# Performance work log

Hardware: AMD Instinct MI355X
Metric: run time of the kernel (lower is better)

## Reference

```python
import jax, jax.numpy as jnp
import numpy as np
from jax.scipy.fft import dct as jdct, idct as jidct

B, C, L = 512, 64, 512
KEEP_L, KEEP_C = 256, 32          # int(L*0.5), int(C*0.5)
KEEP_L2, KEEP_C2 = 128, 16        # int(KEEP_L*0.5), int(KEEP_C*0.5)


def dct2(x2d):
    # scipy: dct(dct(x, axis=0, norm='ortho'), axis=1, norm='ortho') on (B*C, L)
    return jdct(jdct(x2d, norm='ortho', axis=0), norm='ortho', axis=1)


def idct2(x2d):
    # scipy: idct(idct(X, axis=1, norm='ortho'), axis=0, norm='ortho')
    return jidct(jidct(x2d, norm='ortho', axis=1), norm='ortho', axis=0)


def setup_inputs() -> dict:
    key = jax.random.key(0)
    ks = jax.random.split(key, 7)
    x = jax.random.normal(ks[0], (B, C, L), dtype=jnp.float32)
    W1 = jax.random.normal(ks[1], (L, L), dtype=jnp.float32) / np.sqrt(L)
    b1 = jax.random.normal(ks[2], (L,), dtype=jnp.float32) * 0.01
    W2 = jax.random.normal(ks[3], (KEEP_L, KEEP_L), dtype=jnp.float32) / np.sqrt(KEEP_L)
    b2 = jax.random.normal(ks[4], (KEEP_L,), dtype=jnp.float32) * 0.01
    W3 = jax.random.normal(ks[5], (KEEP_L2, KEEP_L2), dtype=jnp.float32) / np.sqrt(KEEP_L2)
    b3 = jax.random.normal(ks[6], (KEEP_L2,), dtype=jnp.float32) * 0.01
    return {"x": x, "W1": W1, "b1": b1, "W2": W2, "b2": b2, "W3": W3, "b3": b3}


def reference(x, W1, b1, W2, b2, W3, b3):
    Bx, Cx, Lx = x.shape
    # 2D DCT over the flattened (B*C, L) view
    T = dct2(x.reshape(-1, Lx)).reshape(Bx, Cx, Lx)

    # branch 1: Linear over full L
    y1 = T @ W1.T + b1

    # branch 2: Linear over truncated coeffs, zero-pad back to (B, C, L)
    t1 = T[:, :KEEP_C, :KEEP_L]
    y2 = jnp.pad(t1 @ W2.T + b2, ((0, 0), (0, Cx - KEEP_C), (0, Lx - KEEP_L)))

    # branch 3: further truncation
    t2 = T[:, :KEEP_C2, :KEEP_L2]
    y3 = jnp.pad(t2 @ W3.T + b3, ((0, 0), (0, Cx - KEEP_C2), (0, Lx - KEEP_L2)))

    out = jnp.concatenate(
        [idct2(y.reshape(-1, Lx)).reshape(Bx, Cx, Lx) for y in (y1, y2, y3)],
        axis=-1,
    )  # (B, C, 3L)
    return out
```

## Files before the change

### kernel.cpp

```cpp
#include <hip/hip_runtime.h>
#include <cstddef>


#define PI_D 3.14159265358979323846

typedef _Float16 h8 __attribute__((ext_vector_type(8)));
typedef _Float16 h4 __attribute__((ext_vector_type(4)));
typedef float f4 __attribute__((ext_vector_type(4)));

#define MFMA16(a, b, c) __builtin_amdgcn_mfma_f32_16x16x32_f16(a, b, c, 0, 0, 0)

__global__ __launch_bounds__(256) void megafill_k(
    float* __restrict__ F, _Float16* __restrict__ Cmh, _Float16* __restrict__ Smnh,
    _Float16* __restrict__ CmTh, _Float16* __restrict__ SmTh,
    float* __restrict__ v1, float* __restrict__ w2, float* __restrict__ w3,
    const float* __restrict__ b1, const float* __restrict__ b2,
    const float* __restrict__ b3, float* __restrict__ c1, float* __restrict__ c2,
    float* __restrict__ c3) {
  const int blk = blockIdx.x;
  const int tid = threadIdx.x;
  if (blk < 1024) {
    int idx = blk * 256 + tid;
    int k = idx >> 9, m = idx & 511;
    int a = (k * (2 * m + 1)) & 2047;
    float ang = (float)(a * (PI_D / 1024.0));
    float s = (k == 0) ? 0.04419417382415922f : 0.0625f;
    F[idx] = s * cosf(ang);
  } else if (blk < 2048) {
    int idx = (blk - 1024) * 256 + tid;
    int t = idx >> 9, v = idx & 511;
    int a = (t * (2 * v + 1)) & 2047;
    float ang = (float)(a * (PI_D / 1024.0));
    float c = cosf(ang), s = sinf(ang);
    Cmh[idx] = (_Float16)c;
    Smnh[idx] = (_Float16)(-s);
    CmTh[v * 512 + t] = (_Float16)c;
    SmTh[v * 512 + t] = (_Float16)s;
  } else if (blk < 2176) {
    int n = (blk - 2048) * 256 + tid;
    const double s1 = 0.005524271728019903;
    const double s2 = 0.0078125;
    double th = (2 * n + 1) * (PI_D / 65536.0);
    double c = cos(th), s = sin(th);
    double Dr = 1.0 - c, Di = -s;
    double dd = Dr * Dr + Di * Di;
    double Nr = 1.0, Ni = (n & 1) ? 1.0 : -1.0;
    double vre = (Nr * Dr + Ni * Di) / dd;
    v1[n] = (float)(s2 * vre + (s1 - s2));
    int m64 = (2 * n + 1) & 2047;
    double a64 = m64 * (PI_D / 1024.0);
    double D64r = 1.0 - cos(a64), D64i = -sin(a64);
    double d64 = D64r * D64r + D64i * D64i;
    double Gr = (Nr * D64r + Ni * D64i) / d64;
    double Gi = (Ni * D64r - Nr * D64i) / d64;
    int m32 = (2 * n + 1) & 4095;
    double a32 = m32 * (PI_D / 2048.0);
    double S32nr = 1.0 - cos(a32), S32ni = -sin(a32);
    double S32r = (S32nr * Dr + S32ni * Di) / dd;
    double S32i = (S32ni * Dr - S32nr * Di) / dd;
    w2[n] = (float)(s2 * (S32r * Gr - S32i * Gi) + (s1 - s2));
    int m16 = (2 * n + 1) & 8191;
    double a16 = m16 * (PI_D / 4096.0);
    double S16nr = 1.0 - cos(a16), S16ni = -sin(a16);
    double S16r = (S16nr * Dr + S16ni * Di) / dd;
    double S16i = (S16ni * Dr - S16nr * Di) / dd;
    w3[n] = (float)(s2 * (S16r * Gr - S16i * Gi) + (s1 - s2));
  } else {
    int gid = (blk - 2176) * 4 + (tid >> 6);
    int lane = tid & 63;
    int branch = gid >> 9;
    int l = gid & 511;
    int K = 512 >> branch;
    const float* b = (branch == 0) ? b1 : (branch == 1) ? b2 : b3;
    float acc = 0.f;
    for (int m = lane; m < K; m += 64) {
      int a = (m * (2 * l + 1)) & 2047;
      float s = (m == 0) ? 0.04419417382415922f : 0.0625f;
      acc += s * cosf((float)(a * (PI_D / 1024.0))) * b[m];
    }
#pragma unroll
    for (int o = 32; o > 0; o >>= 1) acc += __shfl_down(acc, o, 64);
    if (lane == 0) {
      float* c = (branch == 0) ? c1 : (branch == 1) ? c2 : c3;
      c[l] = acc;
    }
  }
}

__global__ void conv_xh_k(const float* __restrict__ X, _Float16* __restrict__ Xh) {
  int i = blockIdx.x * 256 + threadIdx.x;
  float4 v = ((const float4*)X)[i];
  h4 o;
  o[0] = (_Float16)v.x; o[1] = (_Float16)v.y; o[2] = (_Float16)v.z; o[3] = (_Float16)v.w;
  ((h4*)Xh)[i] = o;
}

__device__ void sgemm_dev(_Float16* As, _Float16* Bs, int bx, int by,
                          const float* __restrict__ A, int lda, int transA,
                          const float* __restrict__ B, int ldb,
                          float* __restrict__ Cf, _Float16* __restrict__ C16,
                          int K, float scale) {
  const int tid = threadIdx.x;
  const int lane = tid & 63;
  const int wm = (tid >> 6) & 1, wn = tid >> 7;
  const int m0 = by * 128, n0 = bx * 128;
  const int fm = lane & 15, fko = (lane >> 4) * 8;
  f4 acc[4][4] = {};
  for (int k0 = 0; k0 < K; k0 += 32) {
    if (transA) {
#pragma unroll
      for (int i = 0; i < 4; i++) {
        int idx4 = tid + i * 256;
        int kk = idx4 & 31, mc = (idx4 >> 5) * 4;
        float4 v = *(const float4*)&A[(size_t)(k0 + kk) * lda + m0 + mc];
        As[(mc + 0) * 40 + kk] = (_Float16)v.x;
        As[(mc + 1) * 40 + kk] = (_Float16)v.y;
        As[(mc + 2) * 40 + kk] = (_Float16)v.z;
        As[(mc + 3) * 40 + kk] = (_Float16)v.w;
      }
    } else {
#pragma unroll
      for (int i = 0; i < 4; i++) {
        int idx4 = tid + i * 256;
        int mm = idx4 >> 3, kc = (idx4 & 7) * 4;
        float4 v = *(const float4*)&A[(size_t)(m0 + mm) * lda + k0 + kc];
        h4 o;
        o[0] = (_Float16)v.x; o[1] = (_Float16)v.y; o[2] = (_Float16)v.z; o[3] = (_Float16)v.w;
        *(h4*)&As[mm * 40 + kc] = o;
      }
    }
#pragma unroll
    for (int i = 0; i < 4; i++) {
      int idx4 = tid + i * 256;
      int kk = idx4 & 31, nc = (idx4 >> 5) * 4;
      float4 v = *(const float4*)&B[(size_t)(k0 + kk) * ldb + n0 + nc];
      Bs[(nc + 0) * 40 + kk] = (_Float16)v.x;
      Bs[(nc + 1) * 40 + kk] = (_Float16)v.y;
      Bs[(nc + 2) * 40 + kk] = (_Float16)v.z;
      Bs[(nc + 3) * 40 + kk] = (_Float16)v.w;
    }
    __syncthreads();
    h8 af[4], bf[4];
#pragma unroll
    for (int i = 0; i < 4; i++) af[i] = *(const h8*)&As[(wm * 64 + i * 16 + fm) * 40 + fko];
#pragma unroll
    for (int j = 0; j < 4; j++) bf[j] = *(const h8*)&Bs[(wn * 64 + j * 16 + fm) * 40 + fko];
#pragma unroll
    for (int i = 0; i < 4; i++)
#pragma unroll
      for (int j = 0; j < 4; j++) acc[i][j] = MFMA16(af[i], bf[j], acc[i][j]);
    __syncthreads();
  }
  const int er = (lane >> 4) * 4, ec = lane & 15;
#pragma unroll
  for (int i = 0; i < 4; i++) {
    int gr0 = m0 + wm * 64 + i * 16 + er;
#pragma unroll
    for (int j = 0; j < 4; j++) {
      int gc = n0 + wn * 64 + j * 16 + ec;
#pragma unroll
      for (int r = 0; r < 4; r++) {
        size_t off = (size_t)(gr0 + r) * 512 + gc;
        if (C16) C16[off] = (_Float16)(acc[i][j][r] * scale);
        else Cf[off] = acc[i][j][r];
      }
    }
  }
}

__global__ __launch_bounds__(256) void sgemm_stage1_k(
    const float* __restrict__ W1, const float* __restrict__ W2,
    const float* __restrict__ W3, const float* __restrict__ F,
    float* __restrict__ Pst, float* __restrict__ Q2, float* __restrict__ Q3) {
  __shared__ _Float16 As[128 * 40];
  __shared__ _Float16 Bs[128 * 40];
  int id = blockIdx.x;
  if (id < 16) {
    sgemm_dev(As, Bs, id & 3, id >> 2, W1, 512, 1, F, 512, Pst, nullptr, 512, 1.f);
  } else if (id < 24) {
    int j = id - 16;
    sgemm_dev(As, Bs, j & 3, j >> 2, W2, 256, 0, F, 512, Q2, nullptr, 256, 1.f);
  } else {
    int j = id - 24;
    sgemm_dev(As, Bs, j & 3, j >> 2, W3, 128, 0, F, 512, Q3, nullptr, 128, 1.f);
  }
}

__global__ __launch_bounds__(256) void sgemm_stage2_k(
    const float* __restrict__ F, const float* __restrict__ Pst,
    const float* __restrict__ Q2, const float* __restrict__ Q3,
    _Float16* __restrict__ M1T, _Float16* __restrict__ M2T,
    _Float16* __restrict__ M3T) {
  __shared__ _Float16 As[128 * 40];
  __shared__ _Float16 Bs[128 * 40];
  int id = blockIdx.x;
  if (id < 16) {
    sgemm_dev(As, Bs, id & 3, id >> 2, Pst, 512, 1, F, 512, nullptr, M1T, 512, 1.f);
  } else if (id < 32) {
    int j = id - 16;
    sgemm_dev(As, Bs, j & 3, j >> 2, F, 512, 1, Q2, 512, nullptr, M2T, 256, 0.0078125f);
  } else {
    int j = id - 32;
    sgemm_dev(As, Bs, j & 3, j >> 2, F, 512, 1, Q3, 512, nullptr, M3T, 128, 0.0078125f);
  }
}

__global__ __launch_bounds__(256) void transpose2_h_k(
    const _Float16* __restrict__ in0, _Float16* __restrict__ out0, int C0,
    const _Float16* __restrict__ in1, _Float16* __restrict__ out1, int C1,
    int xsplit, int R) {
  __shared__ _Float16 t[64][66];
  const _Float16* in;
  _Float16* out;
  int C, bx;
  if ((int)blockIdx.x < xsplit) { in = in0; out = out0; C = C0; bx = blockIdx.x; }
  else { in = in1; out = out1; C = C1; bx = blockIdx.x - xsplit; }
  int tid = threadIdx.x;
  int bxo = bx * 64;
  int by = blockIdx.y * 64;
  int cx = (tid & 15) * 4;
  int ry = tid >> 4;
#pragma unroll
  for (int p = 0; p < 4; p++) {
    int r = ry + p * 16;
    h4 v = *(const h4*)&in[(size_t)(by + r) * C + bxo + cx];
    t[r][cx + 0] = v[0]; t[r][cx + 1] = v[1]; t[r][cx + 2] = v[2]; t[r][cx + 3] = v[3];
  }
  __syncthreads();
#pragma unroll
  for (int p = 0; p < 4; p++) {
    int r2 = ry + p * 16;
    h4 v;
    v[0] = t[cx + 0][r2]; v[1] = t[cx + 1][r2]; v[2] = t[cx + 2][r2]; v[3] = t[cx + 3][r2];
    *(h4*)&out[(size_t)(bxo + r2) * R + by + cx] = v;
  }
}

__device__ __forceinline__ void async16(const _Float16* g, _Float16* l) {
  __builtin_amdgcn_global_load_lds((const __attribute__((address_space(1))) void*)g,
                                   (__attribute__((address_space(3))) void*)l, 16, 0, 0);
}

template <int MODE>
__device__ void gemm_dev(_Float16* As, _Float16* Bs, int bx, int by,
                         const _Float16* __restrict__ A1, const _Float16* __restrict__ A2,
                         const _Float16* __restrict__ B1, const _Float16* __restrict__ B2,
                         void* __restrict__ C1, void* __restrict__ C2, int ldc, int coff,
                         const float* __restrict__ u, const float* __restrict__ wvec,
                         int sb, int tb) {
  constexpr bool DA = (MODE == 1 || MODE == 2);
  constexpr bool DB = (MODE == 1);
  const int tid = threadIdx.x;
  const int lane = tid & 63;
  const int wm = (tid >> 6) & 1, wn = tid >> 7;
  const int m0 = by * 128, n0 = bx * 128;
  const int srow = tid >> 2, scol = (tid & 3) * 8;
  const int mask = (1 << sb) - 1;
  f4 acc[4][4] = {};
  f4 acc2[4][4] = {};
  const int fm = lane & 15, fko = (lane >> 4) * 8;
  for (int k0 = 0; k0 < 512; k0 += 32) {
#pragma unroll
    for (int i = 0; i < 2; i++) {
      int r = m0 + i * 64 + srow;
      int pr = ((r >> sb) << tb) | (r & mask);
      async16(A1 + (size_t)pr * 512 + k0 + scol, &As[i * 2048 + tid * 8]);
      if constexpr (DA)
        async16(A2 + (size_t)pr * 512 + k0 + scol, &As[4096 + i * 2048 + tid * 8]);
      int rb = n0 + i * 64 + srow;
      async16(B1 + (size_t)rb * 512 + k0 + scol, &Bs[i * 2048 + tid * 8]);
      if constexpr (DB)
        async16(B2 + (size_t)rb * 512 + k0 + scol, &Bs[4096 + i * 2048 + tid * 8]);
    }
    __syncthreads();
    h8 af[4], bf[4], af2[4], bf2[4];
#pragma unroll
    for (int i = 0; i < 4; i++) {
      int ro = (wm * 64 + i * 16 + fm) * 32 + fko;
      af[i] = *(const h8*)&As[ro];
      if constexpr (DA) af2[i] = *(const h8*)&As[4096 + ro];
    }
#pragma unroll
    for (int j = 0; j < 4; j++) {
      int co = (wn * 64 + j * 16 + fm) * 32 + fko;
      bf[j] = *(const h8*)&Bs[co];
      if constexpr (DB) bf2[j] = *(const h8*)&Bs[4096 + co];
    }
#pragma unroll
    for (int i = 0; i < 4; i++)
#pragma unroll
      for (int j = 0; j < 4; j++) {
        acc[i][j] = MFMA16(af[i], bf[j], acc[i][j]);
        if constexpr (MODE == 1) acc[i][j] = MFMA16(af2[i], bf2[j], acc[i][j]);
        if constexpr (MODE == 2) acc2[i][j] = MFMA16(af2[i], bf[j], acc2[i][j]);
      }
    __syncthreads();
  }
  const int er = (lane >> 4) * 4, ec = lane & 15;
#pragma unroll
  for (int i = 0; i < 4; i++) {
    int gr0 = m0 + wm * 64 + i * 16 + er;
#pragma unroll
    for (int j = 0; j < 4; j++) {
      int gc = n0 + wn * 64 + j * 16 + ec;
#pragma unroll
      for (int r = 0; r < 4; r++) {
        size_t off = (size_t)(gr0 + r) * ldc + coff + gc;
        if constexpr (MODE == 3) {
          ((float*)C1)[off] = acc[i][j][r] + u[gr0 + r] * wvec[gc];
        } else if constexpr (MODE == 2) {
          ((_Float16*)C1)[off] = (_Float16)acc[i][j][r];
          ((_Float16*)C2)[off] = (_Float16)acc2[i][j][r];
        } else if constexpr (MODE == 1) {
          float v = acc[i][j][r];
          if ((gr0 + r) == 0 && gc < 512) v *= 0.5f;
          ((_Float16*)C1)[off] = (_Float16)v;
        } else {
          ((_Float16*)C1)[off] = (_Float16)acc[i][j][r];
        }
      }
    }
  }
}

template <int MODE>
__global__ __launch_bounds__(256) void mfma_gemm_k(
    const _Float16* __restrict__ A1, const _Float16* __restrict__ A2,
    const _Float16* __restrict__ B1, const _Float16* __restrict__ B2,
    void* __restrict__ C1, void* __restrict__ C2, int ldc, int coff,
    const float* __restrict__ u, const float* __restrict__ wvec, int sb, int tb) {
  __shared__ __align__(16) _Float16 As[((MODE == 1 || MODE == 2) ? 2 : 1) * 4096];
  __shared__ __align__(16) _Float16 Bs[(MODE == 1 ? 2 : 1) * 4096];
  gemm_dev<MODE>(As, Bs, blockIdx.x, blockIdx.y, A1, A2, B1, B2, C1, C2, ldc, coff,
                 u, wvec, sb, tb);
}

__global__ __launch_bounds__(256) void gemm_trio_k(
    const _Float16* __restrict__ Zh, const _Float16* __restrict__ M2T,
    const _Float16* __restrict__ M3T, _Float16* __restrict__ Y2,
    _Float16* __restrict__ Y3, const _Float16* __restrict__ Xh,
    const _Float16* __restrict__ M1T, float* __restrict__ out,
    const float* __restrict__ v1, const float* __restrict__ c1) {
  __shared__ __align__(16) _Float16 As[4096];
  __shared__ __align__(16) _Float16 Bs[4096];
  int by = blockIdx.y;
  if (by < 128)
    gemm_dev<0>(As, Bs, blockIdx.x, by, Zh, nullptr, M2T, nullptr, Y2, nullptr,
                512, 0, nullptr, nullptr, 30, 30);
  else if (by < 192)
    gemm_dev<0>(As, Bs, blockIdx.x, by - 128, Zh, nullptr, M3T, nullptr, Y3,
                nullptr, 512, 0, nullptr, nullptr, 4, 5);
  else
    gemm_dev<3>(As, Bs, blockIdx.x, by - 192, Xh, nullptr, M1T, nullptr, out,
                nullptr, 1536, 0, v1, c1, 30, 30);
}

__global__ __launch_bounds__(256) void gemm2_pair_k(
    const _Float16* __restrict__ CmTh, const _Float16* __restrict__ SmTh,
    const _Float16* __restrict__ Y2T, const _Float16* __restrict__ Y3T,
    _Float16* __restrict__ Pc2, _Float16* __restrict__ Ps2,
    _Float16* __restrict__ Pc3, _Float16* __restrict__ Ps3) {
  __shared__ __align__(16) _Float16 As[2 * 4096];
  __shared__ __align__(16) _Float16 Bs[4096];
  if ((int)blockIdx.x < 128)
    gemm_dev<2>(As, Bs, blockIdx.x, blockIdx.y, CmTh, SmTh, Y2T, nullptr, Pc2, Ps2,
                16384, 0, nullptr, nullptr, 30, 30);
  else
    gemm_dev<2>(As, Bs, blockIdx.x - 128, blockIdx.y, CmTh, SmTh, Y3T, nullptr, Pc3,
                Ps3, 8192, 0, nullptr, nullptr, 30, 30);
}

__global__ __launch_bounds__(256) void modmfma_k(
    const _Float16* __restrict__ Xh, _Float16* __restrict__ zc,
    _Float16* __restrict__ zs) {
  __shared__ _Float16 Bs[256 * 72];
  __shared__ _Float16 Ac[32 * 72];
  __shared__ _Float16 As[32 * 72];
  const int tid = threadIdx.x;
  const int lane = tid & 63;
  const int wid = tid >> 6;
  const int vp = blockIdx.y;
  const int l0 = blockIdx.x * 256;
  const float sc = 0.0078125f;
  {
    int r = lane;
    int u = r & 31;
    int n = (r < 32) ? ((u << 10) + vp) : ((u << 10) + 1023 - vp);
    const _Float16* src = Xh + (size_t)n * 512 + l0 + wid * 64;
#pragma unroll
    for (int i = 0; i < 8; i++) {
      h8 v = *(const h8*)(src + i * 8);
      int lb = wid * 64 + i * 8;
#pragma unroll
      for (int e = 0; e < 8; e++) Bs[(lb + e) * 72 + r] = v[e];
    }
  }
  for (int idx = tid; idx < 2048; idx += 256) {
    int kk = idx & 63, j = idx >> 6;
    int u = kk & 31;
    int n = (kk < 32) ? ((u << 10) + vp) : ((u << 10) + 1023 - vp);
    int a = (j * (2 * n + 1)) & 131071;
    float sv, cv;
    __sincosf((float)(a * (PI_D / 65536.0)), &sv, &cv);
    Ac[j * 72 + kk] = (_Float16)(cv * sc);
    As[j * 72 + kk] = (_Float16)(((kk < 32) ? sv : -sv) * sc);
  }
  __syncthreads();
  const int fm = lane & 15, fko = (lane >> 4) * 8;
  f4 accc[2][4] = {};
  f4 accs[2][4] = {};
#pragma unroll
  for (int ks = 0; ks < 2; ks++) {
    int ko = ks * 32 + fko;
    h8 afc[2], afs[2], bf[4];
#pragma unroll
    for (int i = 0; i < 2; i++) {
      afc[i] = *(const h8*)&Ac[(i * 16 + fm) * 72 + ko];
      afs[i] = *(const h8*)&As[(i * 16 + fm) * 72 + ko];
    }
#pragma unroll
    for (int j = 0; j < 4; j++)
      bf[j] = *(const h8*)&Bs[(wid * 64 + j * 16 + fm) * 72 + ko];
#pragma unroll
    for (int i = 0; i < 2; i++)
#pragma unroll
      for (int j = 0; j < 4; j++) {
        accc[i][j] = MFMA16(afc[i], bf[j], accc[i][j]);
        accs[i][j] = MFMA16(afs[i], bf[j], accs[i][j]);
      }
  }
  const int er = (lane >> 4) * 4, ec = lane & 15;
#pragma unroll
  for (int i = 0; i < 2; i++)
#pragma unroll
    for (int j = 0; j < 4; j++)
#pragma unroll
      for (int r = 0; r < 4; r++) {
        int row = i * 16 + er + r;
        int col = l0 + wid * 64 + j * 16 + ec;
        size_t off = (size_t)vp * 16384 + row * 512 + col;
        zc[off] = (_Float16)accc[i][j][r];
        zs[off] = (_Float16)accs[i][j][r];
      }
}

template <int JC>
__device__ void demod_dev(char* smemraw, const _Float16* __restrict__ Pc,
                          const _Float16* __restrict__ Ps,
                          const float* __restrict__ wv, const float* __restrict__ cw,
                          float* __restrict__ out, int coff) {
  constexpr int K2 = 2 * JC;
  constexpr int ST = K2 + 8;
  _Float16* Bs = (_Float16*)smemraw;
  _Float16* At = (_Float16*)(smemraw + (size_t)256 * ST * 2);
  const int tid = threadIdx.x;
  const int lane = tid & 63;
  const int wid = tid >> 6;
  const int vp = blockIdx.y;
  const int l0 = blockIdx.x * 256;
  {
    constexpr int CPL = 64 / K2;
    int r = lane & (K2 - 1);
    int chunk = wid * CPL + (CPL == 1 ? 0 : (lane >> 5));
    int lb = chunk * K2;
    const _Float16* src = (r < JC ? Pc + (size_t)vp * (JC * 512) + r * 512
                                  : Ps + (size_t)vp * (JC * 512) + (r - JC) * 512) +
                          l0 + lb;
#pragma unroll
    for (int i = 0; i < K2 / 8; i++) {
      h8 v = *(const h8*)(src + i * 8);
#pragma unroll
      for (int e = 0; e < 8; e++) Bs[(lb + i * 8 + e) * ST + r] = v[e];
    }
  }
  for (int idx = tid; idx < 64 * K2; idx += 256) {
    int kk = idx & (K2 - 1), m = idx / K2;
    int ab = m >> 5, u = m & 31;
    int n = ab ? ((u << 10) + 1023 - vp) : ((u << 10) + vp);
    int twon = 2 * n + 1;
    float val;
    if (kk < JC) {
      int a = (kk * twon) & 131071;
      val = cosf((float)(a * (PI_D / 65536.0)));
    } else {
      int a = ((kk - JC) * twon) & 131071;
      float sv = sinf((float)(a * (PI_D / 65536.0)));
      val = ab ? sv : -sv;
    }
    At[m * ST + kk] = (_Float16)val;
  }
  __syncthreads();
  const int fm = lane & 15, fko = (lane >> 4) * 8;
  f4 acc[4][4] = {};
#pragma unroll
  for (int ks = 0; ks < K2 / 32; ks++) {
    int ko = ks * 32 + fko;
    h8 af[4], bf[4];
#pragma unroll
    for (int i = 0; i < 4; i++) af[i] = *(const h8*)&At[(i * 16 + fm) * ST + ko];
#pragma unroll
    for (int j = 0; j < 4; j++) bf[j] = *(const h8*)&Bs[(wid * 64 + j * 16 + fm) * ST + ko];
#pragma unroll
    for (int i = 0; i < 4; i++)
#pragma unroll
      for (int j = 0; j < 4; j++) acc[i][j] = MFMA16(af[i], bf[j], acc[i][j]);
  }
  const int er = (lane >> 4) * 4, ec = lane & 15;
#pragma unroll
  for (int i = 0; i < 4; i++)
#pragma unroll
    for (int j = 0; j < 4; j++) {
      int col = l0 + wid * 64 + j * 16 + ec;
      float cl = cw[col];
#pragma unroll
      for (int r = 0; r < 4; r++) {
        int m = i * 16 + er + r;
        int ab = m >> 5, u = m & 31;
        int n = ab ? ((u << 10) + 1023 - vp) : ((u << 10) + vp);
        out[(size_t)n * 1536 + coff + col] = acc[i][j][r] + wv[n] * cl;
      }
    }
}

__global__ __launch_bounds__(256) void demod_pair_k(
    const _Float16* __restrict__ Pc2, const _Float16* __restrict__ Ps2,
    const float* __restrict__ w2v, const float* __restrict__ c2,
    const _Float16* __restrict__ Pc3, const _Float16* __restrict__ Ps3,
    const float* __restrict__ w3v, const float* __restrict__ c3,
    float* __restrict__ out) {
  __shared__ __align__(16) char smem[256 * 72 * 2 + 64 * 72 * 2];
  if (blockIdx.z == 0)
    demod_dev<32>(smem, Pc2, Ps2, w2v, c2, out, 512);
  else
    demod_dev<16>(smem, Pc3, Ps3, w3v, c3, out, 1024);
}

extern "C" void kernel_launch(void* const* d_in, const int* in_sizes, int n_in,
                              void* d_out, int out_size, void* d_ws, size_t ws_size,
                              hipStream_t stream) {
  const float* X  = (const float*)d_in[0];
  const float* W1 = (const float*)d_in[1];
  const float* b1 = (const float*)d_in[2];
  const float* W2 = (const float*)d_in[3];
  const float* b2 = (const float*)d_in[4];
  const float* W3 = (const float*)d_in[5];
  const float* b3 = (const float*)d_in[6];
  float* out = (float*)d_out;
  char* w = (char*)d_ws;
  const size_t MB = 1024 * 1024;

  float* F    = (float*)(w);
  float* v1   = (float*)(w + 9 * MB);
  float* w2v  = (float*)(w + 9 * MB + 131072);
  float* w3v  = (float*)(w + 9 * MB + 262144);
  float* c1   = (float*)(w + 9 * MB + 393216);
  float* c2   = (float*)(w + 9 * MB + 395264);
  float* c3   = (float*)(w + 9 * MB + 397312);
  float* Pst  = (float*)(w + 10 * MB);
  _Float16* CmTh = (_Float16*)(w + 11 * MB);
  _Float16* SmTh = (_Float16*)(w + 11 * MB + 524288);
  _Float16* Cmh  = (_Float16*)(w + 12 * MB);
  _Float16* Smnh = (_Float16*)(w + 12 * MB + 524288);
  _Float16* M1T  = (_Float16*)(w + 13 * MB);
  _Float16* M2T  = (_Float16*)(w + 13 * MB + 524288);
  _Float16* M3T  = (_Float16*)(w + 14 * MB);
  float* Q2      = (float*)(w + 14 * MB + 524288);
  float* Q3      = (float*)(w + 15 * MB);
  _Float16* Xh   = (_Float16*)(w + 16 * MB);
  _Float16* zc   = (_Float16*)(w + 48 * MB);
  _Float16* zs   = (_Float16*)(w + 64 * MB);
  _Float16* Pc2h = (_Float16*)(w + 48 * MB);
  _Float16* Ps2h = (_Float16*)(w + 64 * MB);
  _Float16* Pc3h = (_Float16*)(w + 104 * MB);
  _Float16* Ps3h = (_Float16*)(w + 112 * MB);
  _Float16* zcT  = (_Float16*)(w + 80 * MB);
  _Float16* zsT  = (_Float16*)(w + 96 * MB);
  _Float16* Y2T  = (_Float16*)(w + 80 * MB);
  _Float16* Y3T  = (_Float16*)(w + 96 * MB);
  _Float16* Zh   = (_Float16*)(w + 112 * MB);
  _Float16* Y2   = (_Float16*)(w + 128 * MB);
  _Float16* Y3   = (_Float16*)(w + 144 * MB);

  megafill_k<<<2560, 256, 0, stream>>>(F, Cmh, Smnh, CmTh, SmTh, v1, w2v, w3v,
                                       b1, b2, b3, c1, c2, c3);
  sgemm_stage1_k<<<28, 256, 0, stream>>>(W1, W2, W3, F, Pst, Q2, Q3);
  sgemm_stage2_k<<<48, 256, 0, stream>>>(F, Pst, Q2, Q3, M1T, M2T, M3T);
  conv_xh_k<<<16384, 256, 0, stream>>>(X, Xh);
  modmfma_k<<<dim3(2, 512), 256, 0, stream>>>(Xh, zc, zs);
  transpose2_h_k<<<dim3(512, 8), 256, 0, stream>>>(zc, zcT, 16384, zs, zsT, 16384,
                                                   256, 512);
  mfma_gemm_k<1><<<dim3(128, 4), 256, 0, stream>>>(Cmh, Smnh, zcT, zsT, Zh, nullptr,
                                                   16384, 0, nullptr, nullptr, 30, 30);
  gemm_trio_k<<<dim3(4, 448), 256, 0, stream>>>(Zh, M2T, M3T, Y2, Y3, Xh, M1T, out,
                                                v1, c1);
  transpose2_h_k<<<dim3(384, 8), 256, 0, stream>>>(Y2, Y2T, 16384, Y3, Y3T, 8192,
                                                   256, 512);
  gemm2_pair_k<<<dim3(192, 4), 256, 0, stream>>>(CmTh, SmTh, Y2T, Y3T, Pc2h, Ps2h,
                                                 Pc3h, Ps3h);
  demod_pair_k<<<dim3(2, 512, 2), 256, 0, stream>>>(Pc2h, Ps2h, w2v, c2, Pc3h, Ps3h,
                                                    w3v, c3, out);
}
```

Before: 584.6 us.

## Fuse fp16 conversion into modulation MFMA and co-launch stage-2 sgemm blocks

Drops the standalone float-to-half conversion kernel: the modulation kernel now reads fp32 X directly, converts it in registers, writes Xh for later use and stages it to shared memory. The stage-2 weight sgemm blocks are merged into the same launch as extra blocks, so those independent tasks share one grid and two launches go away. The aim is to cut the extra read of Xh and kernel launch overhead. The fused kernel reads twice as many bytes per element from X and uses a union shared buffer sized for the larger path, which may lower occupancy for the sgemm blocks.

```diff
diff --git a/kernel.cpp b/kernel.cpp
--- a/kernel.cpp
+++ b/kernel.cpp
@@ -87,14 +87,6 @@
   }
 }
 
-__global__ void conv_xh_k(const float* __restrict__ X, _Float16* __restrict__ Xh) {
-  int i = blockIdx.x * 256 + threadIdx.x;
-  float4 v = ((const float4*)X)[i];
-  h4 o;
-  o[0] = (_Float16)v.x; o[1] = (_Float16)v.y; o[2] = (_Float16)v.z; o[3] = (_Float16)v.w;
-  ((h4*)Xh)[i] = o;
-}
-
 __device__ void sgemm_dev(_Float16* As, _Float16* Bs, int bx, int by,
                           const float* __restrict__ A, int lda, int transA,
                           const float* __restrict__ B, int ldb,
@@ -186,22 +178,108 @@
   }
 }
 
-__global__ __launch_bounds__(256) void sgemm_stage2_k(
+__device__ void modmfma_dev(char* smemraw, const float* __restrict__ X,
+                            _Float16* __restrict__ Xh, _Float16* __restrict__ zc,
+                            _Float16* __restrict__ zs, int vp, int l0) {
+  _Float16* Bs = (_Float16*)smemraw;
+  _Float16* Ac = (_Float16*)(smemraw + 36864);
+  _Float16* As = (_Float16*)(smemraw + 41472);
+  const int tid = threadIdx.x;
+  const int lane = tid & 63;
+  const int wid = tid >> 6;
+  const float sc = 0.0078125f;
+  {
+    int r = lane;
+    int u = r & 31;
+    int n = (r < 32) ? ((u << 10) + vp) : ((u << 10) + 1023 - vp);
+    const float* src = X + (size_t)n * 512 + l0 + wid * 64;
+    _Float16* xdst = Xh + (size_t)n * 512 + l0 + wid * 64;
+#pragma unroll
+    for (int i = 0; i < 8; i++) {
+      float4 a = *(const float4*)(src + i * 8);
+      float4 b = *(const float4*)(src + i * 8 + 4);
+      h8 v;
+      v[0] = (_Float16)a.x; v[1] = (_Float16)a.y; v[2] = (_Float16)a.z; v[3] = (_Float16)a.w;
+      v[4] = (_Float16)b.x; v[5] = (_Float16)b.y; v[6] = (_Float16)b.z; v[7] = (_Float16)b.w;
+      *(h8*)(xdst + i * 8) = v;
+      int lb = wid * 64 + i * 8;
+#pragma unroll
+      for (int e = 0; e < 8; e++) Bs[(lb + e) * 72 + r] = v[e];
+    }
+  }
+  for (int idx = tid; idx < 2048; idx += 256) {
+    int kk = idx & 63, j = idx >> 6;
+    int u = kk & 31;
+    int n = (kk < 32) ? ((u << 10) + vp) : ((u << 10) + 1023 - vp);
+    int a = (j * (2 * n + 1)) & 131071;
+    float sv, cv;
+    __sincosf((float)(a * (PI_D / 65536.0)), &sv, &cv);
+    Ac[j * 72 + kk] = (_Float16)(cv * sc);
+    As[j * 72 + kk] = (_Float16)(((kk < 32) ? sv : -sv) * sc);
+  }
+  __syncthreads();
+  const int fm = lane & 15, fko = (lane >> 4) * 8;
+  f4 accc[2][4] = {};
+  f4 accs[2][4] = {};
+#pragma unroll
+  for (int ks = 0; ks < 2; ks++) {
+    int ko = ks * 32 + fko;
+    h8 afc[2], afs[2], bf[4];
+#pragma unroll
+    for (int i = 0; i < 2; i++) {
+      afc[i] = *(const h8*)&Ac[(i * 16 + fm) * 72 + ko];
+      afs[i] = *(const h8*)&As[(i * 16 + fm) * 72 + ko];
+    }
+#pragma unroll
+    for (int j = 0; j < 4; j++)
+      bf[j] = *(const h8*)&Bs[(wid * 64 + j * 16 + fm) * 72 + ko];
+#pragma unroll
+    for (int i = 0; i < 2; i++)
+#pragma unroll
+      for (int j = 0; j < 4; j++) {
+        accc[i][j] = MFMA16(afc[i], bf[j], accc[i][j]);
+        accs[i][j] = MFMA16(afs[i], bf[j], accs[i][j]);
+      }
+  }
+  const int er = (lane >> 4) * 4, ec = lane & 15;
+#pragma unroll
+  for (int i = 0; i < 2; i++)
+#pragma unroll
+    for (int j = 0; j < 4; j++)
+#pragma unroll
+      for (int r = 0; r < 4; r++) {
+        int row = i * 16 + er + r;
+        int col = l0 + wid * 64 + j * 16 + ec;
+        size_t off = (size_t)vp * 16384 + row * 512 + col;
+        zc[off] = (_Float16)accc[i][j][r];
+        zs[off] = (_Float16)accs[i][j][r];
+      }
+}
+
+__global__ __launch_bounds__(256) void mega3_k(
+    const float* __restrict__ X, _Float16* __restrict__ Xh,
+    _Float16* __restrict__ zc, _Float16* __restrict__ zs,
     const float* __restrict__ F, const float* __restrict__ Pst,
     const float* __restrict__ Q2, const float* __restrict__ Q3,
     _Float16* __restrict__ M1T, _Float16* __restrict__ M2T,
     _Float16* __restrict__ M3T) {
-  __shared__ _Float16 As[128 * 40];
-  __shared__ _Float16 Bs[128 * 40];
-  int id = blockIdx.x;
-  if (id < 16) {
-    sgemm_dev(As, Bs, id & 3, id >> 2, Pst, 512, 1, F, 512, nullptr, M1T, 512, 1.f);
-  } else if (id < 32) {
-    int j = id - 16;
-    sgemm_dev(As, Bs, j & 3, j >> 2, F, 512, 1, Q2, 512, nullptr, M2T, 256, 0.0078125f);
+  __shared__ __align__(16) char smem[46080];
+  const int blk = blockIdx.x;
+  if (blk < 1024) {
+    modmfma_dev(smem, X, Xh, zc, zs, blk >> 1, (blk & 1) * 256);
   } else {
-    int j = id - 32;
-    sgemm_dev(As, Bs, j & 3, j >> 2, F, 512, 1, Q3, 512, nullptr, M3T, 128, 0.0078125f);
+    _Float16* As = (_Float16*)smem;
+    _Float16* Bs = (_Float16*)(smem + 128 * 40 * 2);
+    int id = blk - 1024;
+    if (id < 16) {
+      sgemm_dev(As, Bs, id & 3, id >> 2, Pst, 512, 1, F, 512, nullptr, M1T, 512, 1.f);
+    } else if (id < 32) {
+      int j = id - 16;
+      sgemm_dev(As, Bs, j & 3, j >> 2, F, 512, 1, Q2, 512, nullptr, M2T, 256, 0.0078125f);
+    } else {
+      int j = id - 32;
+      sgemm_dev(As, Bs, j & 3, j >> 2, F, 512, 1, Q3, 512, nullptr, M3T, 128, 0.0078125f);
+    }
   }
 }
 
@@ -368,80 +446,6 @@
   else
     gemm_dev<2>(As, Bs, blockIdx.x - 128, blockIdx.y, CmTh, SmTh, Y3T, nullptr, Pc3,
                 Ps3, 8192, 0, nullptr, nullptr, 30, 30);
-}
-
-__global__ __launch_bounds__(256) void modmfma_k(
-    const _Float16* __restrict__ Xh, _Float16* __restrict__ zc,
-    _Float16* __restrict__ zs) {
-  __shared__ _Float16 Bs[256 * 72];
-  __shared__ _Float16 Ac[32 * 72];
-  __shared__ _Float16 As[32 * 72];
-  const int tid = threadIdx.x;
-  const int lane = tid & 63;
-  const int wid = tid >> 6;
-  const int vp = blockIdx.y;
-  const int l0 = blockIdx.x * 256;
-  const float sc = 0.0078125f;
-  {
-    int r = lane;
-    int u = r & 31;
-    int n = (r < 32) ? ((u << 10) + vp) : ((u << 10) + 1023 - vp);
-    const _Float16* src = Xh + (size_t)n * 512 + l0 + wid * 64;
-#pragma unroll
-    for (int i = 0; i < 8; i++) {
-      h8 v = *(const h8*)(src + i * 8);
-      int lb = wid * 64 + i * 8;
-#pragma unroll
-      for (int e = 0; e < 8; e++) Bs[(lb + e) * 72 + r] = v[e];
-    }
-  }
-  for (int idx = tid; idx < 2048; idx += 256) {
-    int kk = idx & 63, j = idx >> 6;
-    int u = kk & 31;
-    int n = (kk < 32) ? ((u << 10) + vp) : ((u << 10) + 1023 - vp);
-    int a = (j * (2 * n + 1)) & 131071;
-    float sv, cv;
-    __sincosf((float)(a * (PI_D / 65536.0)), &sv, &cv);
-    Ac[j * 72 + kk] = (_Float16)(cv * sc);
-    As[j * 72 + kk] = (_Float16)(((kk < 32) ? sv : -sv) * sc);
-  }
-  __syncthreads();
-  const int fm = lane & 15, fko = (lane >> 4) * 8;
-  f4 accc[2][4] = {};
-  f4 accs[2][4] = {};
-#pragma unroll
-  for (int ks = 0; ks < 2; ks++) {
-    int ko = ks * 32 + fko;
-    h8 afc[2], afs[2], bf[4];
-#pragma unroll
-    for (int i = 0; i < 2; i++) {
-      afc[i] = *(const h8*)&Ac[(i * 16 + fm) * 72 + ko];
-      afs[i] = *(const h8*)&As[(i * 16 + fm) * 72 + ko];
-    }
-#pragma unroll
-    for (int j = 0; j < 4; j++)
-      bf[j] = *(const h8*)&Bs[(wid * 64 + j * 16 + fm) * 72 + ko];
-#pragma unroll
-    for (int i = 0; i < 2; i++)
-#pragma unroll
-      for (int j = 0; j < 4; j++) {
-        accc[i][j] = MFMA16(afc[i], bf[j], accc[i][j]);
-        accs[i][j] = MFMA16(afs[i], bf[j], accs[i][j]);
-      }
-  }
-  const int er = (lane >> 4) * 4, ec = lane & 15;
-#pragma unroll
-  for (int i = 0; i < 2; i++)
-#pragma unroll
-    for (int j = 0; j < 4; j++)
-#pragma unroll
-      for (int r = 0; r < 4; r++) {
-        int row = i * 16 + er + r;
-        int col = l0 + wid * 64 + j * 16 + ec;
-        size_t off = (size_t)vp * 16384 + row * 512 + col;
-        zc[off] = (_Float16)accc[i][j][r];
-        zs[off] = (_Float16)accs[i][j][r];
-      }
 }
 
 template <int JC>
@@ -584,9 +588,7 @@
   megafill_k<<<2560, 256, 0, stream>>>(F, Cmh, Smnh, CmTh, SmTh, v1, w2v, w3v,
                                        b1, b2, b3, c1, c2, c3);
   sgemm_stage1_k<<<28, 256, 0, stream>>>(W1, W2, W3, F, Pst, Q2, Q3);
-  sgemm_stage2_k<<<48, 256, 0, stream>>>(F, Pst, Q2, Q3, M1T, M2T, M3T);
-  conv_xh_k<<<16384, 256, 0, stream>>>(X, Xh);
-  modmfma_k<<<dim3(2, 512), 256, 0, stream>>>(Xh, zc, zs);
+  mega3_k<<<1072, 256, 0, stream>>>(X, Xh, zc, zs, F, Pst, Q2, Q3, M1T, M2T, M3T);
   transpose2_h_k<<<dim3(512, 8), 256, 0, stream>>>(zc, zcT, 16384, zs, zsT, 16384,
                                                    256, 512);
   mfma_gemm_k<1><<<dim3(128, 4), 256, 0, stream>>>(Cmh, Smnh, zcT, zsT, Zh, nullptr,
```

Result: slower. 597.0 us (+2.1%).
